# Kernel optimization log

Measured on AMD Instinct MI355X. Metric: run time of the kernel, lower is better.

The kernel has to match this reference:

```python
import jax, jax.numpy as jnp
import numpy as np
from jax import lax

K = 3          # kernel size
PAD = 1        # (K-1)//2
CIN = 256
COUT = 64
NSPLIT = CIN // COUT  # 4
EPS = 1e-5


def _conv2d(x, w, b):
    # x [B,C,H,W], w [O,I,K,K], b [O]
    y = lax.conv_general_dilated(x, w, (1, 1), [(PAD, PAD), (PAD, PAD)],
                                 dimension_numbers=("NCHW", "OIHW", "NCHW"))
    return y + b[None, :, None, None]


def _bilinear_sample(img, py, px):
    # img [C,H,W]; py,px [K2,H,W] absolute sample coords; zero outside borders
    H, W = img.shape[1], img.shape[2]
    y0 = jnp.floor(py)
    x0 = jnp.floor(px)
    wy1 = py - y0
    wx1 = px - x0
    wy0 = 1.0 - wy1
    wx0 = 1.0 - wx1

    def gather(yc, xc):
        valid = (yc >= 0) & (yc <= H - 1) & (xc >= 0) & (xc <= W - 1)
        yi = jnp.clip(yc, 0, H - 1).astype(jnp.int32)
        xi = jnp.clip(xc, 0, W - 1).astype(jnp.int32)
        v = img[:, yi, xi]  # [C,K2,H,W]
        return v * valid.astype(img.dtype)[None]

    return (gather(y0, x0) * (wy0 * wx0)[None]
            + gather(y0, x0 + 1.0) * (wy0 * wx1)[None]
            + gather(y0 + 1.0, x0) * (wy1 * wx0)[None]
            + gather(y0 + 1.0, x0 + 1.0) * (wy1 * wx1)[None])


def _deform_conv(x, offsets, w, b):
    # x [B,C,H,W]; offsets [B,2*K2,H,W] (torchvision layout: per kernel pt (dy,dx));
    # w [O,C,K,K]; b [O]
    B, C, H, W = x.shape
    K2 = K * K
    off = offsets.reshape(B, K2, 2, H, W)
    kh = jnp.arange(K, dtype=x.dtype)
    base_y = (jnp.arange(H, dtype=x.dtype)[None, :, None]
              + (kh[:, None] - PAD).repeat(K).reshape(K2, 1, 1))  # h + kh - pad
    base_x = (jnp.arange(W, dtype=x.dtype)[None, None, :]
              + jnp.tile(kh - PAD, K).reshape(K2, 1, 1))          # w + kw - pad
    py = base_y + off[:, :, 0]  # [B,K2,H,W]
    px = base_x + off[:, :, 1]
    sampled = jax.vmap(_bilinear_sample)(x, py, px)  # [B,C,K2,H,W]
    out = jnp.einsum("bckhw,ock->bohw", sampled, w.reshape(w.shape[0], C, K2))
    return out + b[None, :, None, None]


def setup_inputs() -> dict:
    key = jax.random.key(0)
    ks = jax.random.split(key, 10)
    B, H, W = 8, 64, 64
    x = jax.random.normal(ks[0], (B, CIN, H, W), dtype=jnp.float32)
    bn_gamma = jax.random.normal(ks[1], (CIN,), dtype=jnp.float32) * 0.1 + 1.0
    bn_beta = jax.random.normal(ks[2], (CIN,), dtype=jnp.float32) * 0.1
    bn_mean = jax.random.normal(ks[3], (CIN,), dtype=jnp.float32) * 0.1
    bn_var = jax.random.uniform(ks[4], (CIN,), dtype=jnp.float32, minval=0.5, maxval=1.5)
    offset_w = jax.random.normal(ks[5], (NSPLIT, 2 * K * K, CIN, K, K), dtype=jnp.float32) * 0.02
    offset_b = jax.random.normal(ks[6], (NSPLIT, 2 * K * K), dtype=jnp.float32) * 0.02
    dconv_w = jax.random.normal(ks[7], (NSPLIT, COUT, COUT, K, K), dtype=jnp.float32) * 0.04
    dconv_b = jax.random.normal(ks[8], (NSPLIT, COUT), dtype=jnp.float32) * 0.02
    return {"x": x, "bn_gamma": bn_gamma, "bn_beta": bn_beta, "bn_mean": bn_mean,
            "bn_var": bn_var, "offset_w": offset_w, "offset_b": offset_b,
            "dconv_w": dconv_w, "dconv_b": dconv_b}


def reference(x, bn_gamma, bn_beta, bn_mean, bn_var, offset_w, offset_b, dconv_w, dconv_b):
    # BN (eval-mode running stats) + ReLU
    inv = lax.rsqrt(bn_var + EPS)
    h = jax.nn.relu((x - bn_mean[None, :, None, None]) * (bn_gamma * inv)[None, :, None, None]
                    + bn_beta[None, :, None, None])
    out = None
    for i in range(NSPLIT):
        offsets = _conv2d(h, offset_w[i], offset_b[i])               # [B,2K2,H,W]
        x_i = h[:, i * COUT:(i + 1) * COUT]                          # [B,COUT,H,W]
        y_i = _deform_conv(x_i, offsets, dconv_w[i], dconv_b[i])
        out = y_i if out is None else out + y_i
    return out
```

## Files before the change

### kernel.cpp

```cpp
#include <hip/hip_runtime.h>
#include <hip/hip_bf16.h>

#define KK 3
#define CIN 256
#define COUT 64
#define NSPLIT 4
#define BB 8
#define HH 64
#define WW 64
#define K2 9
#define OC 18
#define EPS 1e-5f
#define HW (HH*WW)

typedef __attribute__((ext_vector_type(8))) short bf16x8;
typedef __attribute__((ext_vector_type(4))) float f32x4;
typedef __attribute__((ext_vector_type(4))) unsigned int u32x4;

#define WS_BSUM  512
#define WS_HBF   1024
#define HBF_FLOATS (BB*HH*WW*CIN/2)
#define WS_OFFS  (WS_HBF + HBF_FLOATS)
#define OFFS_SIZE (BB*72*HH*WW)
#define WS_WDT   (WS_OFFS + OFFS_SIZE)
#define WS_WOB   (WS_WDT + NSPLIT*K2*COUT*COUT/2)
#define WOB_ELEMS (K2*80*CIN)
#define NBN_BLOCKS 2048
#define NWT_BLOCKS ((WOB_ELEMS + 255) / 256)

__device__ __host__ inline unsigned short f2bf(float f) {
    unsigned int u = __builtin_bit_cast(unsigned int, f);
    unsigned int r = (u + 0x7fffu + ((u >> 16) & 1u)) >> 16;
    return (unsigned short)r;
}
__device__ inline float bf2f(unsigned short u) {
    return __builtin_bit_cast(float, (unsigned int)u << 16);
}
__device__ inline unsigned int pkbf(float a, float b) {
    float2 f = {a, b};
    __hip_bfloat162 r = __float22bfloat162_rn(f);
    unsigned int u;
    __builtin_memcpy(&u, &r, 4);
    return u;
}

__global__ __launch_bounds__(256) void prep_kernel(const float* __restrict__ x,
                                                   const float* __restrict__ g,
                                                   const float* __restrict__ be,
                                                   const float* __restrict__ mn,
                                                   const float* __restrict__ vr,
                                                   const float* __restrict__ dw,
                                                   const float* __restrict__ ow,
                                                   const float* __restrict__ db,
                                                   float* __restrict__ ws,
                                                   unsigned short* __restrict__ hbf) {
    if (blockIdx.x < NBN_BLOCKS) {
        __shared__ float tile[64 * 65];
        __shared__ float scl[64], bil[64];
        int bid = blockIdx.x;
        int cg = bid & 3;
        int y  = (bid >> 2) & 63;
        int b  = bid >> 8;
        int t = threadIdx.x;
        if (t < 64) {
            int c = cg * 64 + t;
            float inv = rsqrtf(vr[c] + EPS);
            float sc = g[c] * inv;
            scl[t] = sc;
            bil[t] = be[c] - mn[c] * sc;
        }
        __syncthreads();
        int lane = t & 63;
        int grp  = t >> 6;
        #pragma unroll
        for (int i = 0; i < 16; i++) {
            int cl = grp * 16 + i;
            int c  = cg * 64 + cl;
            float v = x[((b * CIN + c) * HH + y) * WW + lane];
            float h = fmaxf(fmaf(v, scl[cl], bil[cl]), 0.f);
            tile[cl * 65 + lane] = h;
        }
        __syncthreads();
        int cpair = t & 31;
        int pxg   = t >> 5;
        #pragma unroll
        for (int i = 0; i < 8; i++) {
            int px = pxg * 8 + i;
            *(unsigned int*)&hbf[((size_t)(b * HH + y) * WW + px) * CIN + cg * 64 + cpair * 2] =
                pkbf(tile[(cpair * 2) * 65 + px], tile[(cpair * 2 + 1) * 65 + px]);
        }
    } else {
        int tid = (blockIdx.x - NBN_BLOCKS) * 256 + threadIdx.x;
        if (blockIdx.x == NBN_BLOCKS && threadIdx.x < COUT) {
            float s = 0.f;
            for (int i = 0; i < NSPLIT; i++) s += db[i * COUT + threadIdx.x];
            ws[WS_BSUM + threadIdx.x] = s;
        }
        if (tid < NSPLIT * K2 * COUT * COUT) {
            int cin = tid & 63;
            int o = (tid >> 6) & 63;
            int k = (tid / 4096) % 9;
            int s = tid / 36864;
            ((unsigned short*)(ws + WS_WDT))[tid] = f2bf(dw[((s * COUT + o) * COUT + cin) * 9 + k]);
        }
        if (tid < WOB_ELEMS) {
            int cin = tid & 255;
            int sc = (tid >> 8) % 80;
            int k = tid / 20480;
            unsigned short v = 0;
            if (sc < 72) {
                int s = sc / 18, c = sc % 18;
                v = f2bf(ow[((s * OC + c) * CIN + cin) * 9 + k]);
            }
            ((unsigned short*)(ws + WS_WOB))[tid] = v;
        }
    }
}

__global__ __launch_bounds__(256) void offconv_kernel(const unsigned short* __restrict__ hbf,
                                                      const float* __restrict__ offb,
                                                      const unsigned short* __restrict__ woB,
                                                      float* __restrict__ offs_out) {
    __shared__ unsigned short wlds[80 * 264];
    int tid = threadIdx.x;
    int bid = blockIdx.x + 64 * blockIdx.y;
    int b = bid & 7;
    int y = bid >> 3;
    int w  = tid >> 6;
    int l  = tid & 63;
    int lm = l & 15, lk = l >> 4;
    int px = w * 16 + lm;

    f32x4 acc[5];
    #pragma unroll
    for (int nt = 0; nt < 5; nt++) {
        int sc = nt * 16 + lm;
        float ob = (sc < 72) ? offb[sc] : 0.f;
        acc[nt] = (f32x4){ob, ob, ob, ob};
    }
    const unsigned short* hb = hbf + (size_t)b * HH * WW * CIN;
    const bf16x8 zero = {};

    for (int k = 0; k < 9; k++) {
        int dy = k / 3 - 1, dx = k % 3 - 1;
        int ry = y + dy;
        if ((unsigned)ry >= (unsigned)HH) continue;
        __syncthreads();
        const unsigned short* src = woB + (size_t)k * 80 * 256;
        #pragma unroll
        for (int t = 0; t < 10; t++) {
            int idx = tid + t * 256;
            int sc = idx >> 5;
            int co = (idx & 31) * 8;
            *(bf16x8*)&wlds[sc * 264 + co] = *(const bf16x8*)&src[sc * 256 + co];
        }
        __syncthreads();

        int rx = px + dx;
        bool vx = (unsigned)rx < (unsigned)WW;
        const unsigned short* arow = hb + ((size_t)ry * WW + rx) * CIN + lk * 8;
        #pragma unroll
        for (int kt = 0; kt < 8; kt++) {
            bf16x8 a = vx ? *(const bf16x8*)(arow + kt * 32) : zero;
            #pragma unroll
            for (int nt = 0; nt < 5; nt++) {
                bf16x8 bb = *(const bf16x8*)&wlds[(nt * 16 + lm) * 264 + kt * 32 + lk * 8];
                acc[nt] = __builtin_amdgcn_mfma_f32_16x16x32_bf16(a, bb, acc[nt], 0, 0, 0);
            }
        }
    }

    #pragma unroll
    for (int nt = 0; nt < 5; nt++) {
        int sc = nt * 16 + lm;
        if (sc < 72) {
            float4 v = {acc[nt][0], acc[nt][1], acc[nt][2], acc[nt][3]};
            *(float4*)&offs_out[((size_t)(b * 72 + sc) * HH + y) * WW + w * 16 + lk * 4] = v;
        }
    }
}

#define RGN 18432
__global__ __launch_bounds__(512, 4) void deform_kernel(const unsigned short* __restrict__ hbf,
                                                        const float* __restrict__ offp,
                                                        const unsigned short* __restrict__ wdT,
                                                        const float* __restrict__ bsum,
                                                        float* __restrict__ out) {
    __shared__ __align__(16) char lds[2][RGN];

    int tid = threadIdx.x;
    int bid = blockIdx.x + 64 * blockIdx.y;
    int b = bid & 7;
    int y = bid >> 3;

    int h  = tid >> 8;
    int t8 = tid & 255;
    int l  = tid & 63;
    int w4 = t8 >> 6;
    int lm = l & 15;
    int lk = l >> 4;
    int pA = t8 >> 2;
    int cA = t8 & 3;
    int sub = l >> 3;
    int chq = l & 7;

    char* half_ = lds[h];
    char* vbufB = half_;
    char* wbufB = half_ + 8192;
    int2* tbl2  = (int2*)(half_ + 16384);

    f32x4 acc[4];
    #pragma unroll
    for (int nt = 0; nt < 4; nt++) {
        float bs = h ? 0.f : bsum[nt * 16 + lm];
        acc[nt] = (f32x4){bs, bs, bs, bs};
    }

    const unsigned short* hb = hbf + (size_t)b * HH * WW * CIN;
    const float* offbase = offp + ((size_t)(b * 72 + 2 * h * 18) * HH + y) * WW + pA;

    float offy_c = offbase[0];
    float offx_c = offbase[HW];

    for (int it = 0; it < 2 * K2; ++it) {
        int sl = it >= K2;
        int s  = 2 * h + sl;
        int k  = it - sl * K2;

        float offy_n = 0.f, offx_n = 0.f;
        if (it + 1 < 2 * K2) {
            int sl2 = (it + 1) >= K2;
            int k2  = (it + 1) - sl2 * K2;
            const float* oa = offbase + (size_t)(sl2 * 18 + 2 * k2) * HW;
            offy_n = oa[0];
            offx_n = oa[HW];
        }

        const unsigned short* wsrc = wdT + (size_t)((s * 9 + k) * 64) * 64;
        bf16x8 wr0 = *(const bf16x8*)(wsrc + t8 * 16);
        bf16x8 wr1 = *(const bf16x8*)(wsrc + t8 * 16 + 8);

        {
            int dy = k / 3 - 1, dx = k % 3 - 1;
            float py  = (float)(y + dy) + offy_c;
            float px_ = (float)(pA + dx) + offx_c;
            float y0f = floorf(py), x0f = floorf(px_);
            float wy1 = py - y0f, wx1 = px_ - x0f;
            int yt = (int)y0f + (cA >> 1);
            int xt = (int)x0f + (cA & 1);
            float wt = ((cA >> 1) ? wy1 : 1.f - wy1) * ((cA & 1) ? wx1 : 1.f - wx1);
            bool valid = (yt >= 0) && (yt < HH) && (xt >= 0) && (xt < WW);
            wt = valid ? wt : 0.f;
            int yi = min(max(yt, 0), HH - 1);
            int xi = min(max(xt, 0), WW - 1);
            tbl2[pA * 4 + cA] = (int2){yi * WW + xi, __builtin_bit_cast(int, wt)};
        }
        __syncthreads();

        {
            int pg0 = w4 * 16 + sub;
            int pg1 = pg0 + 8;
            float v0[8], v1[8];
            #pragma unroll
            for (int j = 0; j < 8; j++) { v0[j] = 0.f; v1[j] = 0.f; }
            const unsigned short* sb = hb + s * COUT + chq * 8;
            #pragma unroll
            for (int c = 0; c < 4; c++) {
                int2 t0 = tbl2[pg0 * 4 + c];
                int2 t1 = tbl2[pg1 * 4 + c];
                bf16x8 d0 = *(const bf16x8*)(sb + (size_t)t0.x * CIN);
                bf16x8 d1 = *(const bf16x8*)(sb + (size_t)t1.x * CIN);
                float w0 = __builtin_bit_cast(float, t0.y);
                float w1 = __builtin_bit_cast(float, t1.y);
                #pragma unroll
                for (int j = 0; j < 8; j++) {
                    v0[j] = fmaf(w0, bf2f((unsigned short)d0[j]), v0[j]);
                    v1[j] = fmaf(w1, bf2f((unsigned short)d1[j]), v1[j]);
                }
            }
            u32x4 q0, q1;
            #pragma unroll
            for (int j = 0; j < 4; j++) {
                q0[j] = pkbf(v0[2 * j], v0[2 * j + 1]);
                q1[j] = pkbf(v1[2 * j], v1[2 * j + 1]);
            }
            *(u32x4*)(vbufB + pg0 * 128 + ((chq * 16) ^ ((pg0 & 7) << 4))) = q0;
            *(u32x4*)(vbufB + pg1 * 128 + ((chq * 16) ^ ((pg1 & 7) << 4))) = q1;
        }
        {
            int wo = t8 >> 2, wq = t8 & 3;
            int sw = (wo & 7) << 4;
            *(bf16x8*)(wbufB + wo * 128 + ((wq * 32) ^ sw))      = wr0;
            *(bf16x8*)(wbufB + wo * 128 + ((wq * 32 + 16) ^ sw)) = wr1;
        }
        __syncthreads();

        {
            int aswz = (lm & 7) << 4;
            __builtin_amdgcn_s_setprio(1);
            #pragma unroll
            for (int ks = 0; ks < 2; ks++) {
                bf16x8 a = *(const bf16x8*)(vbufB + (w4 * 16 + lm) * 128 +
                                            ((ks * 64 + lk * 16) ^ aswz));
                #pragma unroll
                for (int nt = 0; nt < 4; nt++) {
                    bf16x8 bb = *(const bf16x8*)(wbufB + (nt * 16 + lm) * 128 +
                                                 ((ks * 64 + lk * 16) ^ aswz));
                    acc[nt] = __builtin_amdgcn_mfma_f32_16x16x32_bf16(a, bb, acc[nt], 0, 0, 0);
                }
            }
            __builtin_amdgcn_s_setprio(0);
        }

        offy_c = offy_n;
        offx_c = offx_n;
    }

    __syncthreads();
    float* outT = (float*)half_;
    #pragma unroll
    for (int nt = 0; nt < 4; nt++) {
        *(f32x4*)(&outT[(nt * 16 + lm) * 68 + w4 * 16 + lk * 4]) = acc[nt];
    }
    __syncthreads();
    {
        const float* o0 = (const float*)lds[0];
        const float* o1 = (const float*)lds[1];
        int o = tid >> 3, xp = (tid & 7) * 8;
        float* dst = out + (((size_t)(b * COUT + o)) * HH + y) * WW + xp;
        #pragma unroll
        for (int q = 0; q < 2; q++) {
            float4 a = *(const float4*)(&o0[o * 68 + xp + q * 4]);
            float4 c = *(const float4*)(&o1[o * 68 + xp + q * 4]);
            float4 rr = {a.x + c.x, a.y + c.y, a.z + c.z, a.w + c.w};
            *(float4*)(dst + q * 4) = rr;
        }
    }
}

extern "C" void kernel_launch(void* const* d_in, const int* in_sizes, int n_in,
                              void* d_out, int out_size, void* d_ws, size_t ws_size,
                              hipStream_t stream) {
    const float* x        = (const float*)d_in[0];
    const float* bn_gamma = (const float*)d_in[1];
    const float* bn_beta  = (const float*)d_in[2];
    const float* bn_mean  = (const float*)d_in[3];
    const float* bn_var   = (const float*)d_in[4];
    const float* offset_w = (const float*)d_in[5];
    const float* offset_b = (const float*)d_in[6];
    const float* dconv_w  = (const float*)d_in[7];
    const float* dconv_b  = (const float*)d_in[8];
    float* out = (float*)d_out;
    float* ws  = (float*)d_ws;

    unsigned short* hbf = (unsigned short*)(ws + WS_HBF);

    prep_kernel<<<NBN_BLOCKS + NWT_BLOCKS, 256, 0, stream>>>(x, bn_gamma, bn_beta, bn_mean,
                                                             bn_var, dconv_w, offset_w,
                                                             dconv_b, ws, hbf);
    offconv_kernel<<<dim3(64, 8), 256, 0, stream>>>(hbf, offset_b,
                                                    (const unsigned short*)(ws + WS_WOB),
                                                    ws + WS_OFFS);
    deform_kernel<<<dim3(64, 8), 512, 0, stream>>>(hbf, ws + WS_OFFS,
                                                   (const unsigned short*)(ws + WS_WDT),
                                                   ws + WS_BSUM, out);
}
```

Before: 85.43 us.

## Fuse offset convolution into deformable conv kernel via shared-memory offsets

The separate offset-conv kernel is folded into the deformable-conv kernel. Each block first computes the 72 offset channels for its row with MFMA across 8 waves, split so waves cover 3 or 2 column tiles, and stores them in LDS. The deform stage then reads offsets from LDS instead of global memory. This removes one launch and the global write and read of the offset tensor. In exchange the LDS footprint grows by about 19 KB per block, which may reduce occupancy, and the offset conv now runs serially before the deform work inside each block.

```diff
diff --git a/kernel.cpp b/kernel.cpp
--- a/kernel.cpp
+++ b/kernel.cpp
@@ -20,9 +20,7 @@
 #define WS_BSUM  512
 #define WS_HBF   1024
 #define HBF_FLOATS (BB*HH*WW*CIN/2)
-#define WS_OFFS  (WS_HBF + HBF_FLOATS)
-#define OFFS_SIZE (BB*72*HH*WW)
-#define WS_WDT   (WS_OFFS + OFFS_SIZE)
+#define WS_WDT   (WS_HBF + HBF_FLOATS)
 #define WS_WOB   (WS_WDT + NSPLIT*K2*COUT*COUT/2)
 #define WOB_ELEMS (K2*80*CIN)
 #define NBN_BLOCKS 2048
@@ -117,94 +115,101 @@
     }
 }
 
-__global__ __launch_bounds__(256) void offconv_kernel(const unsigned short* __restrict__ hbf,
-                                                      const float* __restrict__ offb,
-                                                      const unsigned short* __restrict__ woB,
-                                                      float* __restrict__ offs_out) {
-    __shared__ unsigned short wlds[80 * 264];
+#define RGN 18432
+#define OFFS_OFF 42240
+__global__ __launch_bounds__(512, 4) void deform_kernel(const unsigned short* __restrict__ hbf,
+                                                        const unsigned short* __restrict__ wdT,
+                                                        const unsigned short* __restrict__ woB,
+                                                        const float* __restrict__ offb,
+                                                        const float* __restrict__ bsum,
+                                                        float* __restrict__ out) {
+    __shared__ __align__(16) char ldsAll[OFFS_OFF + 72 * 65 * 4];
+
     int tid = threadIdx.x;
     int bid = blockIdx.x + 64 * blockIdx.y;
     int b = bid & 7;
     int y = bid >> 3;
-    int w  = tid >> 6;
+
     int l  = tid & 63;
-    int lm = l & 15, lk = l >> 4;
-    int px = w * 16 + lm;
-
-    f32x4 acc[5];
-    #pragma unroll
-    for (int nt = 0; nt < 5; nt++) {
-        int sc = nt * 16 + lm;
-        float ob = (sc < 72) ? offb[sc] : 0.f;
-        acc[nt] = (f32x4){ob, ob, ob, ob};
-    }
+    int lm = l & 15;
+    int lk = l >> 4;
+
     const unsigned short* hb = hbf + (size_t)b * HH * WW * CIN;
-    const bf16x8 zero = {};
-
-    for (int k = 0; k < 9; k++) {
-        int dy = k / 3 - 1, dx = k % 3 - 1;
-        int ry = y + dy;
-        if ((unsigned)ry >= (unsigned)HH) continue;
-        __syncthreads();
-        const unsigned short* src = woB + (size_t)k * 80 * 256;
-        #pragma unroll
-        for (int t = 0; t < 10; t++) {
-            int idx = tid + t * 256;
-            int sc = idx >> 5;
-            int co = (idx & 31) * 8;
-            *(bf16x8*)&wlds[sc * 264 + co] = *(const bf16x8*)&src[sc * 256 + co];
-        }
-        __syncthreads();
-
-        int rx = px + dx;
-        bool vx = (unsigned)rx < (unsigned)WW;
-        const unsigned short* arow = hb + ((size_t)ry * WW + rx) * CIN + lk * 8;
-        #pragma unroll
-        for (int kt = 0; kt < 8; kt++) {
-            bf16x8 a = vx ? *(const bf16x8*)(arow + kt * 32) : zero;
-            #pragma unroll
-            for (int nt = 0; nt < 5; nt++) {
-                bf16x8 bb = *(const bf16x8*)&wlds[(nt * 16 + lm) * 264 + kt * 32 + lk * 8];
-                acc[nt] = __builtin_amdgcn_mfma_f32_16x16x32_bf16(a, bb, acc[nt], 0, 0, 0);
-            }
-        }
-    }
-
-    #pragma unroll
-    for (int nt = 0; nt < 5; nt++) {
-        int sc = nt * 16 + lm;
-        if (sc < 72) {
-            float4 v = {acc[nt][0], acc[nt][1], acc[nt][2], acc[nt][3]};
-            *(float4*)&offs_out[((size_t)(b * 72 + sc) * HH + y) * WW + w * 16 + lk * 4] = v;
-        }
-    }
-}
-
-#define RGN 18432
-__global__ __launch_bounds__(512, 4) void deform_kernel(const unsigned short* __restrict__ hbf,
-                                                        const float* __restrict__ offp,
-                                                        const unsigned short* __restrict__ wdT,
-                                                        const float* __restrict__ bsum,
-                                                        float* __restrict__ out) {
-    __shared__ __align__(16) char lds[2][RGN];
-
-    int tid = threadIdx.x;
-    int bid = blockIdx.x + 64 * blockIdx.y;
-    int b = bid & 7;
-    int y = bid >> 3;
+    float* offs_ = (float*)(ldsAll + OFFS_OFF);
+
+    {
+        unsigned short* wlds = (unsigned short*)ldsAll;
+        int wv  = tid >> 6;
+        int wm_ = wv & 3;
+        int g2  = wv >> 2;
+        int ntb = g2 ? 3 : 0;
+        int ntn = g2 ? 2 : 3;
+        int px  = wm_ * 16 + lm;
+
+        f32x4 aoc[3];
+        #pragma unroll
+        for (int nt = 0; nt < 3; nt++) {
+            int sc = (ntb + nt) * 16 + lm;
+            float ob = (nt < ntn && sc < 72) ? offb[sc] : 0.f;
+            aoc[nt] = (f32x4){ob, ob, ob, ob};
+        }
+        const bf16x8 zero = {};
+
+        for (int k = 0; k < 9; k++) {
+            int dy = k / 3 - 1, dx = k % 3 - 1;
+            int ry = y + dy;
+            if ((unsigned)ry >= (unsigned)HH) continue;
+            __syncthreads();
+            const unsigned short* src = woB + (size_t)k * 80 * 256;
+            #pragma unroll
+            for (int t = 0; t < 5; t++) {
+                int idx = tid + t * 512;
+                int sc = idx >> 5;
+                int co = (idx & 31) * 8;
+                *(bf16x8*)&wlds[sc * 264 + co] = *(const bf16x8*)&src[sc * 256 + co];
+            }
+            __syncthreads();
+
+            int rx = px + dx;
+            bool vx = (unsigned)rx < (unsigned)WW;
+            const unsigned short* arow = hb + ((size_t)ry * WW + rx) * CIN + lk * 8;
+            #pragma unroll
+            for (int kt = 0; kt < 8; kt++) {
+                bf16x8 a = vx ? *(const bf16x8*)(arow + kt * 32) : zero;
+                #pragma unroll
+                for (int nt = 0; nt < 3; nt++) {
+                    if (nt < ntn) {
+                        bf16x8 bb = *(const bf16x8*)&wlds[((ntb + nt) * 16 + lm) * 264 + kt * 32 + lk * 8];
+                        aoc[nt] = __builtin_amdgcn_mfma_f32_16x16x32_bf16(a, bb, aoc[nt], 0, 0, 0);
+                    }
+                }
+            }
+        }
+
+        #pragma unroll
+        for (int nt = 0; nt < 3; nt++) {
+            if (nt < ntn) {
+                int sc = (ntb + nt) * 16 + lm;
+                if (sc < 72) {
+                    #pragma unroll
+                    for (int j = 0; j < 4; j++) {
+                        offs_[sc * 65 + wm_ * 16 + lk * 4 + j] = aoc[nt][j];
+                    }
+                }
+            }
+        }
+    }
+    __syncthreads();
 
     int h  = tid >> 8;
     int t8 = tid & 255;
-    int l  = tid & 63;
     int w4 = t8 >> 6;
-    int lm = l & 15;
-    int lk = l >> 4;
     int pA = t8 >> 2;
     int cA = t8 & 3;
     int sub = l >> 3;
     int chq = l & 7;
 
-    char* half_ = lds[h];
+    char* half_ = ldsAll + h * RGN;
     char* vbufB = half_;
     char* wbufB = half_ + 8192;
     int2* tbl2  = (int2*)(half_ + 16384);
@@ -216,34 +221,22 @@
         acc[nt] = (f32x4){bs, bs, bs, bs};
     }
 
-    const unsigned short* hb = hbf + (size_t)b * HH * WW * CIN;
-    const float* offbase = offp + ((size_t)(b * 72 + 2 * h * 18) * HH + y) * WW + pA;
-
-    float offy_c = offbase[0];
-    float offx_c = offbase[HW];
-
     for (int it = 0; it < 2 * K2; ++it) {
         int sl = it >= K2;
         int s  = 2 * h + sl;
         int k  = it - sl * K2;
 
-        float offy_n = 0.f, offx_n = 0.f;
-        if (it + 1 < 2 * K2) {
-            int sl2 = (it + 1) >= K2;
-            int k2  = (it + 1) - sl2 * K2;
-            const float* oa = offbase + (size_t)(sl2 * 18 + 2 * k2) * HW;
-            offy_n = oa[0];
-            offx_n = oa[HW];
-        }
-
         const unsigned short* wsrc = wdT + (size_t)((s * 9 + k) * 64) * 64;
         bf16x8 wr0 = *(const bf16x8*)(wsrc + t8 * 16);
         bf16x8 wr1 = *(const bf16x8*)(wsrc + t8 * 16 + 8);
 
         {
+            int plane = s * 18 + 2 * k;
+            float offy = offs_[plane * 65 + pA];
+            float offx = offs_[(plane + 1) * 65 + pA];
             int dy = k / 3 - 1, dx = k % 3 - 1;
-            float py  = (float)(y + dy) + offy_c;
-            float px_ = (float)(pA + dx) + offx_c;
+            float py  = (float)(y + dy) + offy;
+            float px_ = (float)(pA + dx) + offx;
             float y0f = floorf(py), x0f = floorf(px_);
             float wy1 = py - y0f, wx1 = px_ - x0f;
             int yt = (int)y0f + (cA >> 1);
@@ -311,9 +304,6 @@
             }
             __builtin_amdgcn_s_setprio(0);
         }
-
-        offy_c = offy_n;
-        offx_c = offx_n;
     }
 
     __syncthreads();
@@ -324,8 +314,8 @@
     }
     __syncthreads();
     {
-        const float* o0 = (const float*)lds[0];
-        const float* o1 = (const float*)lds[1];
+        const float* o0 = (const float*)(ldsAll);
+        const float* o1 = (const float*)(ldsAll + RGN);
         int o = tid >> 3, xp = (tid & 7) * 8;
         float* dst = out + (((size_t)(b * COUT + o)) * HH + y) * WW + xp;
         #pragma unroll
@@ -358,10 +348,8 @@
     prep_kernel<<<NBN_BLOCKS + NWT_BLOCKS, 256, 0, stream>>>(x, bn_gamma, bn_beta, bn_mean,
                                                              bn_var, dconv_w, offset_w,
                                                              dconv_b, ws, hbf);
-    offconv_kernel<<<dim3(64, 8), 256, 0, stream>>>(hbf, offset_b,
-                                                    (const unsigned short*)(ws + WS_WOB),
-                                                    ws + WS_OFFS);
-    deform_kernel<<<dim3(64, 8), 512, 0, stream>>>(hbf, ws + WS_OFFS,
+    deform_kernel<<<dim3(64, 8), 512, 0, stream>>>(hbf,
                                                    (const unsigned short*)(ws + WS_WDT),
-                                                   ws + WS_BSUM, out);
-}
+                                                   (const unsigned short*)(ws + WS_WOB),
+                                                   offset_b, ws + WS_BSUM, out);
+}
```

After: 91.66 us. 7.3% more time.
